# Performance work log

Hardware: AMD Instinct MI355X
Metric: run time of the kernel (lower is better)

The kernel has to match this reference:

```python
import jax, jax.numpy as jnp
import numpy as np

NUM_CLASSES = 80
NUM_ANCHORS = 3  # len(anchor_mask)
STRIDE = 8.0
# anchors[mask=0,1,2] = (12,16),(19,36),(40,28), divided by stride
ANCHOR_W = jnp.array([12.0, 19.0, 40.0], dtype=jnp.float32) / STRIDE
ANCHOR_H = jnp.array([16.0, 36.0, 28.0], dtype=jnp.float32) / STRIDE


def setup_inputs() -> dict:
    key = jax.random.key(0)
    output = jax.random.normal(key, (16, NUM_ANCHORS * (5 + NUM_CLASSES), 76, 76), dtype=jnp.float32)
    return {"output": output}


def reference(output):
    B, C_total, H, W = output.shape
    A, C = NUM_ANCHORS, NUM_CLASSES
    o = output.reshape(B, A, 5 + C, H, W)

    bxy = jax.nn.sigmoid(o[:, :, 0:2])          # [B,A,2,H,W]
    bwh = jnp.exp(o[:, :, 2:4])                 # [B,A,2,H,W]
    det_confs = jax.nn.sigmoid(o[:, :, 4])      # [B,A,H,W]
    cls_confs = jax.nn.softmax(o[:, :, 5:], axis=2)  # softmax over class dim, [B,A,C,H,W]

    grid_x = jnp.arange(W, dtype=jnp.float32)[None, None, None, :]
    grid_y = jnp.arange(H, dtype=jnp.float32)[None, None, :, None]
    aw = ANCHOR_W[None, :, None, None]
    ah = ANCHOR_H[None, :, None, None]

    bx = (bxy[:, :, 0] + grid_x) / W            # [B,A,H,W]
    by = (bxy[:, :, 1] + grid_y) / H
    bw = (bwh[:, :, 0] * aw) / W
    bh = (bwh[:, :, 1] * ah) / H

    boxes = jnp.stack([bx, by, bw, bh], axis=-1).reshape(B, A * H * W, 4)
    cls_flat = cls_confs.transpose(0, 1, 3, 4, 2).reshape(B, A * H * W, C)
    confs = cls_flat * det_confs.reshape(B, A * H * W, 1)
    return boxes, confs
```

## Files before the change

kernel.cpp:

```cpp
#include <hip/hip_runtime.h>

#define HW_   5776
#define W_    76
#define NC_   80
#define NA_   3
#define NB_   16
#define NCH_  85
#define NPOS  (NB_ * NA_ * HW_)

__device__ __forceinline__ float sigmoidf_(float x) {
    return 1.0f / (1.0f + __expf(-x));
}

__global__ __launch_bounds__(256) void yolo_kernel(const float* __restrict__ in,
                                                   float* __restrict__ out) {
    const int tid  = threadIdx.x;
    const int lane = tid & 63;
    const int wv   = tid >> 6;
    const int half = lane >> 5;
    const int P = blockIdx.x * 128 + wv * 32 + (lane & 31);

    const int slab = P / HW_;
    const int p    = P - slab * HW_;
    const int a    = slab % NA_;

    const float aw3[3] = {1.5f, 2.375f, 5.0f};
    const float ah3[3] = {2.0f, 4.5f, 3.5f};
    const float invW = 1.0f / 76.0f;

    const float* src = in + (size_t)slab * (NCH_ * HW_) + p;

    const float b0 = src[0 * (size_t)HW_];
    const float b1 = src[1 * (size_t)HW_];
    const float b2 = src[2 * (size_t)HW_];
    const float b3 = src[3 * (size_t)HW_];
    const float b4 = src[4 * (size_t)HW_];

    const float* csrc = src + (size_t)(5 + half * 40) * HW_;
    float v[40];
#pragma unroll
    for (int c = 0; c < 40; ++c) v[c] = csrc[(size_t)c * HW_];

    const int x = p % W_;
    const int y = p / W_;
    const float bx  = (sigmoidf_(b0) + (float)x) * invW;
    const float by  = (sigmoidf_(b1) + (float)y) * invW;
    const float bw  = __expf(b2) * (aw3[a] * invW);
    const float bh  = __expf(b3) * (ah3[a] * invW);
    const float det = sigmoidf_(b4);

    float m = v[0];
#pragma unroll
    for (int c = 1; c < 40; ++c) m = fmaxf(m, v[c]);
    m = fmaxf(m, __shfl_xor(m, 32));
    float s = 0.0f;
#pragma unroll
    for (int c = 0; c < 40; ++c) { v[c] = __expf(v[c] - m); s += v[c]; }
    s += __shfl_xor(s, 32);
    const float scale = det / s;

    if (half == 0) {
        ((float4*)out)[P] = make_float4(bx, by, bw, bh);
    }
    float* conf = out + (size_t)NPOS * 4 + (size_t)P * NC_ + half * 40;
#pragma unroll
    for (int c = 0; c < 40; c += 4) {
        *(float4*)(conf + c) = make_float4(v[c]     * scale,
                                           v[c + 1] * scale,
                                           v[c + 2] * scale,
                                           v[c + 3] * scale);
    }
}

extern "C" void kernel_launch(void* const* d_in, const int* in_sizes, int n_in,
                              void* d_out, int out_size, void* d_ws, size_t ws_size,
                              hipStream_t stream) {
    const float* in = (const float*)d_in[0];
    float* out = (float*)d_out;
    const int nblocks = NPOS / 128;
    yolo_kernel<<<nblocks, 256, 0, stream>>>(in, out);
}
```

Measured before the change: 184.7 us.

## Process two positions per thread and stage confidence stores through LDS for coalescing

Each thread now handles two adjacent spatial positions and loads them as float2, halving the block size while covering the same 128 positions per block. The class-confidence output is transposed through a swizzled shared-memory buffer so each wave writes contiguous float4 runs, instead of each lane writing 160-byte strided chunks. This targets global write coalescing and load width. The cost is doubled register pressure from 80 floats per thread, extra LDS traffic, and a serialized four-step staging loop. The code relies on wave-level LDS ordering with no explicit barriers.

```diff
diff --git a/kernel.cpp b/kernel.cpp
--- a/kernel.cpp
+++ b/kernel.cpp
@@ -5,70 +5,112 @@
 #define NC_   80
 #define NA_   3
 #define NB_   16
-#define NCH_  85
 #define NPOS  (NB_ * NA_ * HW_)
+#define ROWQ  24
 
 __device__ __forceinline__ float sigmoidf_(float x) {
     return 1.0f / (1.0f + __expf(-x));
 }
 
-__global__ __launch_bounds__(256) void yolo_kernel(const float* __restrict__ in,
-                                                   float* __restrict__ out) {
+__global__ __launch_bounds__(128, 4) void yolo_kernel(const float* __restrict__ in,
+                                                      float* __restrict__ out) {
+    __shared__ float4 lds[2][16 * ROWQ];
+
     const int tid  = threadIdx.x;
     const int lane = tid & 63;
     const int wv   = tid >> 6;
     const int half = lane >> 5;
-    const int P = blockIdx.x * 128 + wv * 32 + (lane & 31);
+    const int pair = lane & 31;
 
-    const int slab = P / HW_;
-    const int p    = P - slab * HW_;
+    const int waveP0 = blockIdx.x * 128 + wv * 64;
+    const int P0     = waveP0 + pair * 2;
+
+    const int slab = P0 / HW_;
+    const int p    = P0 - slab * HW_;
     const int a    = slab % NA_;
 
     const float aw3[3] = {1.5f, 2.375f, 5.0f};
     const float ah3[3] = {2.0f, 4.5f, 3.5f};
     const float invW = 1.0f / 76.0f;
 
-    const float* src = in + (size_t)slab * (NCH_ * HW_) + p;
+    const float* src = in + (size_t)slab * (85 * (size_t)HW_) + p;
 
-    const float b0 = src[0 * (size_t)HW_];
-    const float b1 = src[1 * (size_t)HW_];
-    const float b2 = src[2 * (size_t)HW_];
-    const float b3 = src[3 * (size_t)HW_];
-    const float b4 = src[4 * (size_t)HW_];
+    const float2 b0 = *(const float2*)(src + 0 * (size_t)HW_);
+    const float2 b1 = *(const float2*)(src + 1 * (size_t)HW_);
+    const float2 b2 = *(const float2*)(src + 2 * (size_t)HW_);
+    const float2 b3 = *(const float2*)(src + 3 * (size_t)HW_);
+    const float2 b4 = *(const float2*)(src + 4 * (size_t)HW_);
 
     const float* csrc = src + (size_t)(5 + half * 40) * HW_;
-    float v[40];
+    float2 v[40];
 #pragma unroll
-    for (int c = 0; c < 40; ++c) v[c] = csrc[(size_t)c * HW_];
+    for (int c = 0; c < 40; ++c) v[c] = *(const float2*)(csrc + (size_t)c * HW_);
 
-    const int x = p % W_;
-    const int y = p / W_;
-    const float bx  = (sigmoidf_(b0) + (float)x) * invW;
-    const float by  = (sigmoidf_(b1) + (float)y) * invW;
-    const float bw  = __expf(b2) * (aw3[a] * invW);
-    const float bh  = __expf(b3) * (ah3[a] * invW);
-    const float det = sigmoidf_(b4);
+    const int x0 = p % W_;
+    const int y0 = p / W_;
+    const int wrap = (x0 == W_ - 1);
+    const int x1 = wrap ? 0 : x0 + 1;
+    const int y1 = y0 + wrap;
 
-    float m = v[0];
+    const float bx0 = (sigmoidf_(b0.x) + (float)x0) * invW;
+    const float by0 = (sigmoidf_(b1.x) + (float)y0) * invW;
+    const float bw0 = __expf(b2.x) * (aw3[a] * invW);
+    const float bh0 = __expf(b3.x) * (ah3[a] * invW);
+    const float d0  = sigmoidf_(b4.x);
+    const float bx1 = (sigmoidf_(b0.y) + (float)x1) * invW;
+    const float by1 = (sigmoidf_(b1.y) + (float)y1) * invW;
+    const float bw1 = __expf(b2.y) * (aw3[a] * invW);
+    const float bh1 = __expf(b3.y) * (ah3[a] * invW);
+    const float d1  = sigmoidf_(b4.y);
+
+    float m0 = v[0].x, m1 = v[0].y;
 #pragma unroll
-    for (int c = 1; c < 40; ++c) m = fmaxf(m, v[c]);
-    m = fmaxf(m, __shfl_xor(m, 32));
-    float s = 0.0f;
+    for (int c = 1; c < 40; ++c) { m0 = fmaxf(m0, v[c].x); m1 = fmaxf(m1, v[c].y); }
+    m0 = fmaxf(m0, __shfl_xor(m0, 32));
+    m1 = fmaxf(m1, __shfl_xor(m1, 32));
+    float s0 = 0.0f, s1 = 0.0f;
 #pragma unroll
-    for (int c = 0; c < 40; ++c) { v[c] = __expf(v[c] - m); s += v[c]; }
-    s += __shfl_xor(s, 32);
-    const float scale = det / s;
+    for (int c = 0; c < 40; ++c) {
+        v[c].x = __expf(v[c].x - m0); s0 += v[c].x;
+        v[c].y = __expf(v[c].y - m1); s1 += v[c].y;
+    }
+    s0 += __shfl_xor(s0, 32);
+    s1 += __shfl_xor(s1, 32);
+    const float sc0 = d0 / s0;
+    const float sc1 = d1 / s1;
 
     if (half == 0) {
-        ((float4*)out)[P] = make_float4(bx, by, bw, bh);
+        float4* out4 = (float4*)out;
+        out4[P0]     = make_float4(bx0, by0, bw0, bh0);
+        out4[P0 + 1] = make_float4(bx1, by1, bw1, bh1);
     }
-    float* conf = out + (size_t)NPOS * 4 + (size_t)P * NC_ + half * 40;
+
+    float4* conf4 = (float4*)out + NPOS + (size_t)waveP0 * 20;
+    const int myt = pair >> 3;
+    const int lp0 = (pair & 7) * 2;
 #pragma unroll
-    for (int c = 0; c < 40; c += 4) {
-        *(float4*)(conf + c) = make_float4(v[c]     * scale,
-                                           v[c + 1] * scale,
-                                           v[c + 2] * scale,
-                                           v[c + 3] * scale);
+    for (int t = 0; t < 4; ++t) {
+        if (myt == t) {
+#pragma unroll
+            for (int i = 0; i < 10; ++i) {
+                const int k = half * 10 + i;
+                const int sl0 = lp0 * ROWQ + (k ^ (lp0 & 7));
+                lds[wv][sl0] = make_float4(v[4*i].x * sc0, v[4*i+1].x * sc0,
+                                           v[4*i+2].x * sc0, v[4*i+3].x * sc0);
+                const int lp1 = lp0 + 1;
+                const int sl1 = lp1 * ROWQ + (k ^ (lp1 & 7));
+                lds[wv][sl1] = make_float4(v[4*i].y * sc1, v[4*i+1].y * sc1,
+                                           v[4*i+2].y * sc1, v[4*i+3].y * sc1);
+            }
+        }
+#pragma unroll
+        for (int i = 0; i < 5; ++i) {
+            const int f    = i * 64 + lane;
+            const int lp   = f / 20;
+            const int kq   = f - lp * 20;
+            const int slot = lp * ROWQ + (kq ^ (lp & 7));
+            conf4[t * 320 + f] = lds[wv][slot];
+        }
     }
 }
 
@@ -78,5 +120,5 @@
     const float* in = (const float*)d_in[0];
     float* out = (float*)d_out;
     const int nblocks = NPOS / 128;
-    yolo_kernel<<<nblocks, 256, 0, stream>>>(in, out);
+    yolo_kernel<<<nblocks, 128, 0, stream>>>(in, out);
 }
```

Result: faster. 179.0 us (-3.1%).
